# Optimization experiments

Hardware: AMD Instinct MI355X
Metric: run time of the kernel (lower is better)

## Reference

```python
import jax, jax.numpy as jnp
import numpy as np

N = 50000      # nodes
E = 800000     # edges (before self loops)
H = 4          # heads
C_IN = 128     # input feature dim
C_HID = 64     # per-head out channels (hidden_dim == output_dim)
SLOPE = 0.2    # GATConv leaky_relu negative slope


def setup_inputs() -> dict:
    key = jax.random.key(0)
    ks = jax.random.split(key, 16)
    x = jax.random.normal(ks[0], (N, C_IN), jnp.float32)
    edge_index = jax.random.randint(ks[1], (2, E), 0, N, jnp.int32)

    def p(k, shape):
        return jax.random.normal(k, shape, jnp.float32) * 0.05

    inp = {"x": x, "edge_index": edge_index}
    in_dims = [C_IN, C_HID, C_HID]
    for i in range(3):
        inp[f"W{i+1}"] = p(ks[2 + 4 * i], (in_dims[i], H * C_HID))
        inp[f"asrc{i+1}"] = p(ks[3 + 4 * i], (H, C_HID))
        inp[f"adst{i+1}"] = p(ks[4 + 4 * i], (H, C_HID))
        inp[f"b{i+1}"] = jnp.zeros((C_HID,), jnp.float32)
    return inp


def _gat_layer(x, src, dst, W, a_s, a_d, b):
    # x: [N, F_in]; src/dst: [E'] (self loops included)
    n = x.shape[0]
    h = (x @ W).reshape(n, H, -1)                      # [N, H, C]
    alpha_src = jnp.einsum('nhc,hc->nh', h, a_s)       # att_src . h  (source side)
    alpha_dst = jnp.einsum('nhc,hc->nh', h, a_d)       # att_dst . h  (target side)
    e = jax.nn.leaky_relu(alpha_src[src] + alpha_dst[dst], SLOPE)  # [E', H]
    # scatter-softmax over incoming edges of each dst node
    m = jax.ops.segment_max(e, dst, num_segments=n)    # [N, H]
    ex = jnp.exp(e - m[dst])
    denom = jax.ops.segment_sum(ex, dst, num_segments=n)
    alpha = ex / (denom[dst] + 1e-16)                  # [E', H]
    # scatter-add aggregation of weighted source features
    out = jax.ops.segment_sum(alpha[:, :, None] * h[src], dst, num_segments=n)  # [N, H, C]
    return out.mean(axis=1) + b                        # concat=False -> head mean, + bias


def reference(x, edge_index, W1, asrc1, adst1, b1, W2, asrc2, adst2, b2,
              W3, asrc3, adst3, b3):
    n = x.shape[0]
    loops = jnp.arange(n, dtype=edge_index.dtype)      # GATConv add_self_loops=True
    src = jnp.concatenate([edge_index[0], loops])
    dst = jnp.concatenate([edge_index[1], loops])
    for W, a_s, a_d, b in ((W1, asrc1, adst1, b1),
                           (W2, asrc2, adst2, b2),
                           (W3, asrc3, adst3, b3)):
        x = jax.nn.relu(_gat_layer(x, src, dst, W, a_s, a_d, b))
    return x
```

## Files before the change

kernel.cpp:

```cpp
#include <hip/hip_runtime.h>
#include <hip/hip_bf16.h>
#include <cstddef>

#define NH 4
#define CHID 64
#define HC 256

typedef __attribute__((ext_vector_type(8))) short bf16x8;
typedef __attribute__((ext_vector_type(4))) float f32x4;


__global__ void hist_kernel(const int* __restrict__ ei, int E, int N,
                            int* __restrict__ deg) {
  int i = blockIdx.x * blockDim.x + threadIdx.x;
  int EP = E + N;
  if (i >= EP) return;
  int d = (i < E) ? ei[E + i] : (i - E);
  atomicAdd(&deg[d], 1);
}

__global__ __launch_bounds__(256) void partial_sum_kernel(const int* __restrict__ deg,
                                                          int* __restrict__ part, int n) {
  __shared__ int red[4];
  int t = threadIdx.x;
  int i = blockIdx.x * 256 + t;
  int v = (i < n) ? deg[i] : 0;
#pragma unroll
  for (int o = 32; o; o >>= 1) v += __shfl_xor(v, o, 64);
  if ((t & 63) == 0) red[t >> 6] = v;
  __syncthreads();
  if (t == 0) part[blockIdx.x] = red[0] + red[1] + red[2] + red[3];
}

__global__ __launch_bounds__(256) void scan_part_kernel(int* __restrict__ part, int nb,
                                                        int* __restrict__ row_off, int n) {
  __shared__ int s[256];
  int t = threadIdx.x;
  int v = (t < nb) ? part[t] : 0;
  s[t] = v;
  __syncthreads();
  for (int o = 1; o < 256; o <<= 1) {
    int u = (t >= o) ? s[t - o] : 0;
    __syncthreads();
    s[t] += u;
    __syncthreads();
  }
  if (t < nb) part[t] = s[t] - v;
  if (t == 255) row_off[n] = s[255];
}

__global__ __launch_bounds__(256) void row_off_kernel(const int* __restrict__ deg,
                                                      const int* __restrict__ part,
                                                      int* __restrict__ row_off, int n) {
  __shared__ int s[256];
  int t = threadIdx.x;
  int i = blockIdx.x * 256 + t;
  int v = (i < n) ? deg[i] : 0;
  s[t] = v;
  __syncthreads();
  for (int o = 1; o < 256; o <<= 1) {
    int u = (t >= o) ? s[t - o] : 0;
    __syncthreads();
    s[t] += u;
    __syncthreads();
  }
  if (i < n) row_off[i] = part[blockIdx.x] + s[t] - v;
}

__global__ void scatter_kernel(const int* __restrict__ ei, int E, int N,
                               const int* __restrict__ row_off,
                               int* __restrict__ cursor, int* __restrict__ ssrc,
                               int* __restrict__ sdst) {
  int i = blockIdx.x * blockDim.x + threadIdx.x;
  int EP = E + N;
  if (i >= EP) {
    if (i < EP + 8) { ssrc[i] = 0; sdst[i] = 0; }
    return;
  }
  int s, d;
  if (i < E) { s = ei[i]; d = ei[E + i]; } else { s = i - E; d = s; }
  int pos = row_off[d] + atomicAdd(&cursor[d], 1);
  ssrc[pos] = s;
  sdst[pos] = d;
}


__global__ void split_x_kernel(const float* __restrict__ x,
                               __hip_bfloat16* __restrict__ hi,
                               __hip_bfloat16* __restrict__ lo, int n4) {
  int i = blockIdx.x * blockDim.x + threadIdx.x;
  if (i >= n4) return;
  float4 v = reinterpret_cast<const float4*>(x)[i];
  __hip_bfloat16 h[4], l[4];
  float f[4] = {v.x, v.y, v.z, v.w};
#pragma unroll
  for (int j = 0; j < 4; ++j) {
    h[j] = __float2bfloat16(f[j]);
    l[j] = __float2bfloat16(f[j] - __bfloat162float(h[j]));
  }
  reinterpret_cast<uint2*>(hi)[i] = *reinterpret_cast<uint2*>(h);
  reinterpret_cast<uint2*>(lo)[i] = *reinterpret_cast<uint2*>(l);
}

__global__ void split_wt3_kernel(const float* __restrict__ W1, const float* __restrict__ W2,
                                 const float* __restrict__ W3,
                                 __hip_bfloat16* __restrict__ w1hi,
                                 __hip_bfloat16* __restrict__ w2hi,
                                 __hip_bfloat16* __restrict__ w3hi) {
  int i = blockIdx.x * blockDim.x + threadIdx.x;
  const float* W; __hip_bfloat16* hi; int K, base;
  if (i < 32768)      { W = W1; hi = w1hi; K = 128; base = i; }
  else if (i < 49152) { W = W2; hi = w2hi; K = 64;  base = i - 32768; }
  else                { W = W3; hi = w3hi; K = 64;  base = i - 49152; }
  int k = base >> 8;
  int c = base & 255;
  hi[c * K + k] = __float2bfloat16(W[base]);
}


__global__ __launch_bounds__(256) void gemm_mfma_kernel(
    const __hip_bfloat16* __restrict__ Ahi, const __hip_bfloat16* __restrict__ Alo,
    const __hip_bfloat16* __restrict__ Bthi,
    const float* __restrict__ a_s, const float* __restrict__ a_d,
    __hip_bfloat16* __restrict__ h, float* __restrict__ asrc_n,
    float* __restrict__ adst_n, int n_rows, int K, int row_groups) {
  extern __shared__ char smem[];
  uint4* lds4 = reinterpret_cast<uint4*>(smem);
  const int S16 = (256 * K * 2) >> 4;
  const int rowshift = (K == 128) ? 4 : 3;

  {
    const uint4* g_hi = reinterpret_cast<const uint4*>(Bthi);
    for (int c = threadIdx.x; c < S16; c += 256) {
      int row = c >> rowshift;
      lds4[c ^ (row & 7)] = g_hi[c];
    }
  }
  __syncthreads();

  int wave = threadIdx.x >> 6;
  int lane = threadIdx.x & 63;
  int n16  = lane & 15;
  int g4   = lane >> 4;
  const bf16x8 z8 = {0, 0, 0, 0, 0, 0, 0, 0};

  for (int g = blockIdx.x; g < row_groups; g += gridDim.x) {
    int row0 = g * 64 + wave * 16;
    int xrow = row0 + n16;
    bool aval = xrow < n_rows;
    size_t xbase = (size_t)xrow * K + g4 * 8;

    f32x4 acc[16];
#pragma unroll
    for (int ct = 0; ct < 16; ++ct) acc[ct] = (f32x4){0.f, 0.f, 0.f, 0.f};

    for (int k0 = 0; k0 < K; k0 += 32) {
      bf16x8 xh = aval ? *reinterpret_cast<const bf16x8*>(&Ahi[xbase + k0]) : z8;
      bf16x8 xl = aval ? *reinterpret_cast<const bf16x8*>(&Alo[xbase + k0]) : z8;
#pragma unroll
      for (int ct = 0; ct < 16; ++ct) {
        int wrow = ct * 16 + n16;
        int ci = ((wrow * K + k0 + g4 * 8) >> 3) ^ (wrow & 7);
        bf16x8 wh = *reinterpret_cast<const bf16x8*>(&lds4[ci]);
        acc[ct] = __builtin_amdgcn_mfma_f32_16x16x32_bf16(wh, xh, acc[ct], 0, 0, 0);
        acc[ct] = __builtin_amdgcn_mfma_f32_16x16x32_bf16(wh, xl, acc[ct], 0, 0, 0);
      }
    }

    int r = row0 + n16;
    bool valid = r < n_rows;

    if (valid) {
#pragma unroll
      for (int ct = 0; ct < 16; ++ct) {
        unsigned short u[4];
#pragma unroll
        for (int i = 0; i < 4; ++i) {
          __hip_bfloat16 b = __float2bfloat16(acc[ct][i]);
          u[i] = *reinterpret_cast<unsigned short*>(&b);
        }
        *reinterpret_cast<uint2*>(&h[(size_t)r * HC + ct * 16 + g4 * 4]) =
            *reinterpret_cast<uint2*>(u);
      }
    }

    float ps[NH] = {0.f, 0.f, 0.f, 0.f};
    float pd[NH] = {0.f, 0.f, 0.f, 0.f};
#pragma unroll
    for (int ct = 0; ct < 16; ++ct) {
      int hh = ct >> 2;
      float4 as4 = *reinterpret_cast<const float4*>(&a_s[ct * 16 + g4 * 4]);
      float4 ad4 = *reinterpret_cast<const float4*>(&a_d[ct * 16 + g4 * 4]);
      ps[hh] += acc[ct][0] * as4.x + acc[ct][1] * as4.y + acc[ct][2] * as4.z + acc[ct][3] * as4.w;
      pd[hh] += acc[ct][0] * ad4.x + acc[ct][1] * ad4.y + acc[ct][2] * ad4.z + acc[ct][3] * ad4.w;
    }
#pragma unroll
    for (int hh = 0; hh < NH; ++hh) {
      ps[hh] += __shfl_xor(ps[hh], 16, 64);
      ps[hh] += __shfl_xor(ps[hh], 32, 64);
      pd[hh] += __shfl_xor(pd[hh], 16, 64);
      pd[hh] += __shfl_xor(pd[hh], 32, 64);
    }
    if (lane < 16 && valid) {
      *reinterpret_cast<float4*>(&asrc_n[(size_t)r * NH]) =
          make_float4(ps[0], ps[1], ps[2], ps[3]);
      *reinterpret_cast<float4*>(&adst_n[(size_t)r * NH]) =
          make_float4(pd[0], pd[1], pd[2], pd[3]);
    }
  }
}


__global__ void edge_weight_kernel(const int* __restrict__ ssrc, const int* __restrict__ sdst,
                                   const float* __restrict__ asrc_n,
                                   const float* __restrict__ adst_n,
                                   float4* __restrict__ wbuf, int EP) {
  int i = blockIdx.x * blockDim.x + threadIdx.x;
  if (i >= EP) {
    if (i < EP + 8) wbuf[i] = make_float4(0.f, 0.f, 0.f, 0.f);
    return;
  }
  int s = ssrc[i];
  int d = sdst[i];
  float4 a = reinterpret_cast<const float4*>(asrc_n)[s];
  float4 b = reinterpret_cast<const float4*>(adst_n)[d];
  float e0 = a.x + b.x; e0 = (e0 > 0.f) ? e0 : 0.2f * e0;
  float e1 = a.y + b.y; e1 = (e1 > 0.f) ? e1 : 0.2f * e1;
  float e2 = a.z + b.z; e2 = (e2 > 0.f) ? e2 : 0.2f * e2;
  float e3 = a.w + b.w; e3 = (e3 > 0.f) ? e3 : 0.2f * e3;
  wbuf[i] = make_float4(__expf(e0), __expf(e1), __expf(e2), __expf(e3));
}


__global__ __launch_bounds__(256) void aggregate_kernel(
    const int* __restrict__ row_off, const int* __restrict__ ssrc,
    const __hip_bfloat16* __restrict__ h, const float4* __restrict__ wbuf,
    const float* __restrict__ bias,
    __hip_bfloat16* __restrict__ out_hi, __hip_bfloat16* __restrict__ out_lo,
    float* __restrict__ out_f32, int n_nodes) {
  int wid    = (blockIdx.x * blockDim.x + threadIdx.x) >> 6;
  int nwaves = (gridDim.x * blockDim.x) >> 6;
  int l    = threadIdx.x & 63;
  int slot = l >> 3;
  int cp   = l & 7;
  const char* hbase = reinterpret_cast<const char*>(h);
  const float4 z4 = make_float4(0.f, 0.f, 0.f, 0.f);
  const uint4 zu = {0, 0, 0, 0};

  for (int n = wid; n < n_nodes; n += nwaves) {
    int beg  = row_off[n];
    int deg  = row_off[n + 1] - beg;

    float facc[32];
#pragma unroll
    for (int u = 0; u < 32; ++u) facc[u] = 0.f;
    float4 ds = z4;

    auto LOADE = [&](int j, float4& w4, uint4* d) {
      int jj  = j + slot;
      int idx = beg + jj;
      int sv  = ssrc[idx];
      float4 w = wbuf[idx];
      bool ok = jj < deg;
      w4.x = ok ? w.x : 0.f;
      w4.y = ok ? w.y : 0.f;
      w4.z = ok ? w.z : 0.f;
      w4.w = ok ? w.w : 0.f;
      const char* hp = hbase + (size_t)sv * 512 + cp * 16;
      d[0] = *reinterpret_cast<const uint4*>(hp);
      d[1] = *reinterpret_cast<const uint4*>(hp + 128);
      d[2] = *reinterpret_cast<const uint4*>(hp + 256);
      d[3] = *reinterpret_cast<const uint4*>(hp + 384);
    };

    auto PROC = [&](const float4& w4, const uint4* d) {
      ds.x += w4.x; ds.y += w4.y; ds.z += w4.z; ds.w += w4.w;
#pragma unroll
      for (int hh = 0; hh < 4; ++hh) {
        float w = (hh == 0) ? w4.x : (hh == 1) ? w4.y : (hh == 2) ? w4.z : w4.w;
        uint4 dd = d[hh];
        facc[hh * 8 + 0] += w * __uint_as_float(dd.x << 16);
        facc[hh * 8 + 1] += w * __uint_as_float(dd.x & 0xffff0000u);
        facc[hh * 8 + 2] += w * __uint_as_float(dd.y << 16);
        facc[hh * 8 + 3] += w * __uint_as_float(dd.y & 0xffff0000u);
        facc[hh * 8 + 4] += w * __uint_as_float(dd.z << 16);
        facc[hh * 8 + 5] += w * __uint_as_float(dd.z & 0xffff0000u);
        facc[hh * 8 + 6] += w * __uint_as_float(dd.w << 16);
        facc[hh * 8 + 7] += w * __uint_as_float(dd.w & 0xffff0000u);
      }
    };

    float4 wA = z4, wB = z4;
    uint4 dA[4] = {zu, zu, zu, zu};
    uint4 dB[4] = {zu, zu, zu, zu};

    LOADE(0, wA, dA);
    for (int j = 0; j < deg; j += 16) {
      if (j + 8 < deg) LOADE(j + 8, wB, dB); else wB = z4;
      PROC(wA, dA);
      if (j + 16 < deg) LOADE(j + 16, wA, dA); else wA = z4;
      PROC(wB, dB);
    }

#pragma unroll
    for (int o = 8; o <= 32; o <<= 1) {
      ds.x += __shfl_xor(ds.x, o, 64);
      ds.y += __shfl_xor(ds.y, o, 64);
      ds.z += __shfl_xor(ds.z, o, 64);
      ds.w += __shfl_xor(ds.w, o, 64);
    }
    float iv0 = 1.f / (ds.x + 1e-16f);
    float iv1 = 1.f / (ds.y + 1e-16f);
    float iv2 = 1.f / (ds.z + 1e-16f);
    float iv3 = 1.f / (ds.w + 1e-16f);

    float v[8];
#pragma unroll
    for (int u = 0; u < 8; ++u)
      v[u] = facc[u] * iv0 + facc[8 + u] * iv1 + facc[16 + u] * iv2 + facc[24 + u] * iv3;

#pragma unroll
    for (int u = 0; u < 8; ++u) {
      v[u] += __shfl_xor(v[u], 8, 64);
      v[u] += __shfl_xor(v[u], 16, 64);
      v[u] += __shfl_xor(v[u], 32, 64);
    }

    if (slot < 2) {
      float o0 = (slot == 0) ? v[0] : v[4];
      float o1 = (slot == 0) ? v[1] : v[5];
      float o2 = (slot == 0) ? v[2] : v[6];
      float o3 = (slot == 0) ? v[3] : v[7];
      int ch = cp * 8 + slot * 4;
      float4 b4 = *reinterpret_cast<const float4*>(&bias[ch]);
      o0 = fmaxf(0.25f * o0 + b4.x, 0.f);
      o1 = fmaxf(0.25f * o1 + b4.y, 0.f);
      o2 = fmaxf(0.25f * o2 + b4.z, 0.f);
      o3 = fmaxf(0.25f * o3 + b4.w, 0.f);
      if (out_f32) {
        *reinterpret_cast<float4*>(&out_f32[(size_t)n * CHID + ch]) =
            make_float4(o0, o1, o2, o3);
      } else {
        float of[4] = {o0, o1, o2, o3};
        unsigned short hi4[4], lo4[4];
#pragma unroll
        for (int u = 0; u < 4; ++u) {
          __hip_bfloat16 bh = __float2bfloat16(of[u]);
          hi4[u] = *reinterpret_cast<unsigned short*>(&bh);
          __hip_bfloat16 bl = __float2bfloat16(of[u] - __bfloat162float(bh));
          lo4[u] = *reinterpret_cast<unsigned short*>(&bl);
        }
        *reinterpret_cast<uint2*>(&out_hi[(size_t)n * CHID + ch]) = *reinterpret_cast<uint2*>(hi4);
        *reinterpret_cast<uint2*>(&out_lo[(size_t)n * CHID + ch]) = *reinterpret_cast<uint2*>(lo4);
      }
    }
  }
}


extern "C" void kernel_launch(void* const* d_in, const int* in_sizes, int n_in,
                              void* d_out, int out_size, void* d_ws, size_t ws_size,
                              hipStream_t stream) {
  const float* x   = (const float*)d_in[0];
  const int*   ei  = (const int*)d_in[1];
  const float* W1  = (const float*)d_in[2];
  const float* as1 = (const float*)d_in[3];
  const float* ad1 = (const float*)d_in[4];
  const float* b1  = (const float*)d_in[5];
  const float* W2  = (const float*)d_in[6];
  const float* as2 = (const float*)d_in[7];
  const float* ad2 = (const float*)d_in[8];
  const float* b2  = (const float*)d_in[9];
  const float* W3  = (const float*)d_in[10];
  const float* as3 = (const float*)d_in[11];
  const float* ad3 = (const float*)d_in[12];
  const float* b3  = (const float*)d_in[13];

  int N  = in_sizes[0] / 128;
  int E  = in_sizes[1] / 2;
  int EP = E + N;
  int NB = (N + 255) / 256;

  __hip_bfloat16* h     = (__hip_bfloat16*)d_ws;
  __hip_bfloat16* x1hi  = h + (size_t)N * HC;
  __hip_bfloat16* x1lo  = x1hi + (size_t)N * 128;
  __hip_bfloat16* xhi   = x1lo + (size_t)N * 128;
  __hip_bfloat16* xlo   = xhi + (size_t)N * CHID;
  __hip_bfloat16* w1hi  = xlo + (size_t)N * CHID;
  __hip_bfloat16* w2hi  = w1hi + 256 * 128;
  __hip_bfloat16* w3hi  = w2hi + 256 * 64;
  float* asrc_n = (float*)(w3hi + 256 * 64);
  float* adst_n = asrc_n + (size_t)N * NH;
  float4* wbuf  = (float4*)(adst_n + (size_t)N * NH);
  int*   deg    = (int*)(wbuf + (EP + 8));
  int*   cursor = deg + N;
  int*   row_off= cursor + N;
  int*   part   = row_off + (N + 1);
  int*   ssrc   = part + ((NB + 3) & ~3);
  int*   sdst   = ssrc + (EP + 8);

  hipMemsetAsync(deg, 0, sizeof(int) * (size_t)2 * N, stream);
  int eb = (EP + 8 + 255) / 256;
  hist_kernel<<<eb, 256, 0, stream>>>(ei, E, N, deg);
  partial_sum_kernel<<<NB, 256, 0, stream>>>(deg, part, N);
  scan_part_kernel<<<1, 256, 0, stream>>>(part, NB, row_off, N);
  row_off_kernel<<<NB, 256, 0, stream>>>(deg, part, row_off, N);
  scatter_kernel<<<eb, 256, 0, stream>>>(ei, E, N, row_off, cursor, ssrc, sdst);

  split_x_kernel<<<(N * 128 / 4 + 255) / 256, 256, 0, stream>>>(x, x1hi, x1lo, N * 128 / 4);
  split_wt3_kernel<<<(65536 + 255) / 256, 256, 0, stream>>>(W1, W2, W3, w1hi, w2hi, w3hi);

  (void)hipFuncSetAttribute(reinterpret_cast<const void*>(gemm_mfma_kernel),
                            hipFuncAttributeMaxDynamicSharedMemorySize, 131072);

  int RG = (N + 63) / 64;
  int ablocks = 1024;

  gemm_mfma_kernel<<<RG, 256, 65536, stream>>>(x1hi, x1lo, w1hi, as1, ad1,
                                               h, asrc_n, adst_n, N, 128, RG);
  edge_weight_kernel<<<eb, 256, 0, stream>>>(ssrc, sdst, asrc_n, adst_n, wbuf, EP);
  aggregate_kernel<<<ablocks, 256, 0, stream>>>(row_off, ssrc, h, wbuf, b1,
                                                xhi, xlo, nullptr, N);
  gemm_mfma_kernel<<<RG, 256, 32768, stream>>>(xhi, xlo, w2hi, as2, ad2,
                                               h, asrc_n, adst_n, N, 64, RG);
  edge_weight_kernel<<<eb, 256, 0, stream>>>(ssrc, sdst, asrc_n, adst_n, wbuf, EP);
  aggregate_kernel<<<ablocks, 256, 0, stream>>>(row_off, ssrc, h, wbuf, b2,
                                                xhi, xlo, nullptr, N);
  gemm_mfma_kernel<<<RG, 256, 32768, stream>>>(xhi, xlo, w3hi, as3, ad3,
                                               h, asrc_n, adst_n, N, 64, RG);
  edge_weight_kernel<<<eb, 256, 0, stream>>>(ssrc, sdst, asrc_n, adst_n, wbuf, EP);
  aggregate_kernel<<<ablocks, 256, 0, stream>>>(row_off, ssrc, h, wbuf, b3,
                                                nullptr, nullptr, (float*)d_out, N);
}
```

Measured before the change: 417.6 us.

## Split GEMM output columns across grid y, template on K, raise aggregate blocks

The MFMA GEMM is templated on K and splits the 256 output columns into two 128-column halves via blockIdx.y. Each block stages only half the weights in LDS, which halves the shared memory footprint, and keeps 8 accumulators instead of 16, so more blocks and waves can be resident. Each half writes two heads' attention logits. The A rows are preloaded for all K steps up front, and the aggregate kernel block count doubles. In exchange, A tiles are read twice, once per column half.

```diff
diff --git a/kernel.cpp b/kernel.cpp
--- a/kernel.cpp
+++ b/kernel.cpp
@@ -118,22 +118,26 @@
 }
 
 
+template <int K>
 __global__ __launch_bounds__(256) void gemm_mfma_kernel(
     const __hip_bfloat16* __restrict__ Ahi, const __hip_bfloat16* __restrict__ Alo,
     const __hip_bfloat16* __restrict__ Bthi,
     const float* __restrict__ a_s, const float* __restrict__ a_d,
     __hip_bfloat16* __restrict__ h, float* __restrict__ asrc_n,
-    float* __restrict__ adst_n, int n_rows, int K, int row_groups) {
+    float* __restrict__ adst_n, int n_rows, int row_groups) {
   extern __shared__ char smem[];
   uint4* lds4 = reinterpret_cast<uint4*>(smem);
-  const int S16 = (256 * K * 2) >> 4;
-  const int rowshift = (K == 128) ? 4 : 3;
+  constexpr int KS = K / 32;
+  constexpr int S16 = (128 * K * 2) >> 4;
+  constexpr int rowshift = (K == 128) ? 4 : 3;
+  int ch = blockIdx.y;
+  int colbase = ch * 128;
 
   {
-    const uint4* g_hi = reinterpret_cast<const uint4*>(Bthi);
+    const uint4* g = reinterpret_cast<const uint4*>(Bthi + (size_t)colbase * K);
     for (int c = threadIdx.x; c < S16; c += 256) {
       int row = c >> rowshift;
-      lds4[c ^ (row & 7)] = g_hi[c];
+      lds4[c ^ (row & 7)] = g[c];
     }
   }
   __syncthreads();
@@ -144,26 +148,32 @@
   int g4   = lane >> 4;
   const bf16x8 z8 = {0, 0, 0, 0, 0, 0, 0, 0};
 
-  for (int g = blockIdx.x; g < row_groups; g += gridDim.x) {
-    int row0 = g * 64 + wave * 16;
+  for (int gg = blockIdx.x; gg < row_groups; gg += gridDim.x) {
+    int row0 = gg * 64 + wave * 16;
     int xrow = row0 + n16;
     bool aval = xrow < n_rows;
     size_t xbase = (size_t)xrow * K + g4 * 8;
 
-    f32x4 acc[16];
-#pragma unroll
-    for (int ct = 0; ct < 16; ++ct) acc[ct] = (f32x4){0.f, 0.f, 0.f, 0.f};
-
-    for (int k0 = 0; k0 < K; k0 += 32) {
-      bf16x8 xh = aval ? *reinterpret_cast<const bf16x8*>(&Ahi[xbase + k0]) : z8;
-      bf16x8 xl = aval ? *reinterpret_cast<const bf16x8*>(&Alo[xbase + k0]) : z8;
-#pragma unroll
-      for (int ct = 0; ct < 16; ++ct) {
-        int wrow = ct * 16 + n16;
-        int ci = ((wrow * K + k0 + g4 * 8) >> 3) ^ (wrow & 7);
+    bf16x8 xh[KS], xl[KS];
+#pragma unroll
+    for (int s = 0; s < KS; ++s) {
+      xh[s] = aval ? *reinterpret_cast<const bf16x8*>(&Ahi[xbase + s * 32]) : z8;
+      xl[s] = aval ? *reinterpret_cast<const bf16x8*>(&Alo[xbase + s * 32]) : z8;
+    }
+
+    f32x4 acc[8];
+#pragma unroll
+    for (int ct = 0; ct < 8; ++ct) acc[ct] = (f32x4){0.f, 0.f, 0.f, 0.f};
+
+#pragma unroll
+    for (int ct = 0; ct < 8; ++ct) {
+      int wrow = ct * 16 + n16;
+#pragma unroll
+      for (int s = 0; s < KS; ++s) {
+        int ci = ((wrow * K + s * 32 + g4 * 8) >> 3) ^ (wrow & 7);
         bf16x8 wh = *reinterpret_cast<const bf16x8*>(&lds4[ci]);
-        acc[ct] = __builtin_amdgcn_mfma_f32_16x16x32_bf16(wh, xh, acc[ct], 0, 0, 0);
-        acc[ct] = __builtin_amdgcn_mfma_f32_16x16x32_bf16(wh, xl, acc[ct], 0, 0, 0);
+        acc[ct] = __builtin_amdgcn_mfma_f32_16x16x32_bf16(wh, xh[s], acc[ct], 0, 0, 0);
+        acc[ct] = __builtin_amdgcn_mfma_f32_16x16x32_bf16(wh, xl[s], acc[ct], 0, 0, 0);
       }
     }
 
@@ -172,40 +182,41 @@
 
     if (valid) {
 #pragma unroll
-      for (int ct = 0; ct < 16; ++ct) {
+      for (int ct = 0; ct < 8; ++ct) {
         unsigned short u[4];
 #pragma unroll
         for (int i = 0; i < 4; ++i) {
           __hip_bfloat16 b = __float2bfloat16(acc[ct][i]);
           u[i] = *reinterpret_cast<unsigned short*>(&b);
         }
-        *reinterpret_cast<uint2*>(&h[(size_t)r * HC + ct * 16 + g4 * 4]) =
+        *reinterpret_cast<uint2*>(&h[(size_t)r * HC + colbase + ct * 16 + g4 * 4]) =
             *reinterpret_cast<uint2*>(u);
       }
     }
 
-    float ps[NH] = {0.f, 0.f, 0.f, 0.f};
-    float pd[NH] = {0.f, 0.f, 0.f, 0.f};
-#pragma unroll
-    for (int ct = 0; ct < 16; ++ct) {
+    float ps[2] = {0.f, 0.f};
+    float pd[2] = {0.f, 0.f};
+#pragma unroll
+    for (int ct = 0; ct < 8; ++ct) {
       int hh = ct >> 2;
-      float4 as4 = *reinterpret_cast<const float4*>(&a_s[ct * 16 + g4 * 4]);
-      float4 ad4 = *reinterpret_cast<const float4*>(&a_d[ct * 16 + g4 * 4]);
+      int col = colbase + ct * 16 + g4 * 4;
+      float4 as4 = *reinterpret_cast<const float4*>(&a_s[col]);
+      float4 ad4 = *reinterpret_cast<const float4*>(&a_d[col]);
       ps[hh] += acc[ct][0] * as4.x + acc[ct][1] * as4.y + acc[ct][2] * as4.z + acc[ct][3] * as4.w;
       pd[hh] += acc[ct][0] * ad4.x + acc[ct][1] * ad4.y + acc[ct][2] * ad4.z + acc[ct][3] * ad4.w;
     }
 #pragma unroll
-    for (int hh = 0; hh < NH; ++hh) {
+    for (int hh = 0; hh < 2; ++hh) {
       ps[hh] += __shfl_xor(ps[hh], 16, 64);
       ps[hh] += __shfl_xor(ps[hh], 32, 64);
       pd[hh] += __shfl_xor(pd[hh], 16, 64);
       pd[hh] += __shfl_xor(pd[hh], 32, 64);
     }
     if (lane < 16 && valid) {
-      *reinterpret_cast<float4*>(&asrc_n[(size_t)r * NH]) =
-          make_float4(ps[0], ps[1], ps[2], ps[3]);
-      *reinterpret_cast<float4*>(&adst_n[(size_t)r * NH]) =
-          make_float4(pd[0], pd[1], pd[2], pd[3]);
+      *reinterpret_cast<float2*>(&asrc_n[(size_t)r * NH + ch * 2]) =
+          make_float2(ps[0], ps[1]);
+      *reinterpret_cast<float2*>(&adst_n[(size_t)r * NH + ch * 2]) =
+          make_float2(pd[0], pd[1]);
     }
   }
 }
@@ -331,14 +342,14 @@
       float o1 = (slot == 0) ? v[1] : v[5];
       float o2 = (slot == 0) ? v[2] : v[6];
       float o3 = (slot == 0) ? v[3] : v[7];
-      int ch = cp * 8 + slot * 4;
-      float4 b4 = *reinterpret_cast<const float4*>(&bias[ch]);
+      int chn = cp * 8 + slot * 4;
+      float4 b4 = *reinterpret_cast<const float4*>(&bias[chn]);
       o0 = fmaxf(0.25f * o0 + b4.x, 0.f);
       o1 = fmaxf(0.25f * o1 + b4.y, 0.f);
       o2 = fmaxf(0.25f * o2 + b4.z, 0.f);
       o3 = fmaxf(0.25f * o3 + b4.w, 0.f);
       if (out_f32) {
-        *reinterpret_cast<float4*>(&out_f32[(size_t)n * CHID + ch]) =
+        *reinterpret_cast<float4*>(&out_f32[(size_t)n * CHID + chn]) =
             make_float4(o0, o1, o2, o3);
       } else {
         float of[4] = {o0, o1, o2, o3};
@@ -350,8 +361,8 @@
           __hip_bfloat16 bl = __float2bfloat16(of[u] - __bfloat162float(bh));
           lo4[u] = *reinterpret_cast<unsigned short*>(&bl);
         }
-        *reinterpret_cast<uint2*>(&out_hi[(size_t)n * CHID + ch]) = *reinterpret_cast<uint2*>(hi4);
-        *reinterpret_cast<uint2*>(&out_lo[(size_t)n * CHID + ch]) = *reinterpret_cast<uint2*>(lo4);
+        *reinterpret_cast<uint2*>(&out_hi[(size_t)n * CHID + chn]) = *reinterpret_cast<uint2*>(hi4);
+        *reinterpret_cast<uint2*>(&out_lo[(size_t)n * CHID + chn]) = *reinterpret_cast<uint2*>(lo4);
       }
     }
   }
@@ -410,24 +421,27 @@
   split_x_kernel<<<(N * 128 / 4 + 255) / 256, 256, 0, stream>>>(x, x1hi, x1lo, N * 128 / 4);
   split_wt3_kernel<<<(65536 + 255) / 256, 256, 0, stream>>>(W1, W2, W3, w1hi, w2hi, w3hi);
 
-  (void)hipFuncSetAttribute(reinterpret_cast<const void*>(gemm_mfma_kernel),
-                            hipFuncAttributeMaxDynamicSharedMemorySize, 131072);
+  (void)hipFuncSetAttribute(reinterpret_cast<const void*>(&gemm_mfma_kernel<128>),
+                            hipFuncAttributeMaxDynamicSharedMemorySize, 65536);
+  (void)hipFuncSetAttribute(reinterpret_cast<const void*>(&gemm_mfma_kernel<64>),
+                            hipFuncAttributeMaxDynamicSharedMemorySize, 65536);
 
   int RG = (N + 63) / 64;
-  int ablocks = 1024;
-
-  gemm_mfma_kernel<<<RG, 256, 65536, stream>>>(x1hi, x1lo, w1hi, as1, ad1,
-                                               h, asrc_n, adst_n, N, 128, RG);
+  dim3 ggrid(RG, 2);
+  int ablocks = 2048;
+
+  gemm_mfma_kernel<128><<<ggrid, 256, 32768, stream>>>(x1hi, x1lo, w1hi, as1, ad1,
+                                                       h, asrc_n, adst_n, N, RG);
   edge_weight_kernel<<<eb, 256, 0, stream>>>(ssrc, sdst, asrc_n, adst_n, wbuf, EP);
   aggregate_kernel<<<ablocks, 256, 0, stream>>>(row_off, ssrc, h, wbuf, b1,
                                                 xhi, xlo, nullptr, N);
-  gemm_mfma_kernel<<<RG, 256, 32768, stream>>>(xhi, xlo, w2hi, as2, ad2,
-                                               h, asrc_n, adst_n, N, 64, RG);
+  gemm_mfma_kernel<64><<<ggrid, 256, 16384, stream>>>(xhi, xlo, w2hi, as2, ad2,
+                                                      h, asrc_n, adst_n, N, RG);
   edge_weight_kernel<<<eb, 256, 0, stream>>>(ssrc, sdst, asrc_n, adst_n, wbuf, EP);
   aggregate_kernel<<<ablocks, 256, 0, stream>>>(row_off, ssrc, h, wbuf, b2,
                                                 xhi, xlo, nullptr, N);
-  gemm_mfma_kernel<<<RG, 256, 32768, stream>>>(xhi, xlo, w3hi, as3, ad3,
-                                               h, asrc_n, adst_n, N, 64, RG);
+  gemm_mfma_kernel<64><<<ggrid, 256, 16384, stream>>>(xhi, xlo, w3hi, as3, ad3,
+                                                      h, asrc_n, adst_n, N, RG);
   edge_weight_kernel<<<eb, 256, 0, stream>>>(ssrc, sdst, asrc_n, adst_n, wbuf, EP);
   aggregate_kernel<<<ablocks, 256, 0, stream>>>(row_off, ssrc, h, wbuf, b3,
                                                 nullptr, nullptr, (float*)d_out, N);
```

Result: no change. 411.0 us (-1.6%).
